# Optimization experiments

Measured on AMD Instinct MI355X. Metric: run time of the kernel, lower is better.

## Reference

```python
import jax, jax.numpy as jnp
import numpy as np
from jax import lax


def _crf_numerator(emissions, tags, mask, start_transitions, end_transitions, transitions):
    # emissions [B,S,L], tags [B,S] int, mask [B,S] bool
    B, S, L = emissions.shape
    em = jnp.take_along_axis(emissions, tags[..., None], axis=-1)[..., 0]  # [B,S]
    tr = transitions[tags[:, :-1], tags[:, 1:]]  # [B,S-1]
    m = mask.astype(emissions.dtype)
    score = start_transitions[tags[:, 0]] + em[:, 0]
    score = score + jnp.sum(m[:, 1:] * (tr + em[:, 1:]), axis=1)
    seq_len = jnp.sum(mask.astype(jnp.int32), axis=1)  # [B]
    last_tags = tags[jnp.arange(B), seq_len - 1]
    return score + end_transitions[last_tags]


def _crf_denominator(emissions, mask, start_transitions, end_transitions, transitions):
    # Forward algorithm (log-sum-exp recurrence) over time via lax.scan.
    score0 = start_transitions[None, :] + emissions[:, 0]  # [B,L]

    def step(score, inp):
        emit, m = inp  # emit [B,L], m [B] bool
        nxt = jax.nn.logsumexp(score[:, :, None] + transitions[None, :, :] + emit[:, None, :], axis=1)
        score = jnp.where(m[:, None], nxt, score)
        return score, None

    emits = jnp.swapaxes(emissions[:, 1:], 0, 1)  # [S-1,B,L]
    ms = jnp.swapaxes(mask[:, 1:], 0, 1)          # [S-1,B]
    score, _ = lax.scan(step, score0, (emits, ms))
    return jax.nn.logsumexp(score + end_transitions[None, :], axis=1)


def setup_inputs() -> dict:
    key = jax.random.key(0)
    ks = jax.random.split(key, 6)
    B, S, H, L = 32, 2048, 1024, 13
    hidden_states = jax.random.normal(ks[0], (B, S, H), jnp.float32)
    attention_mask = jnp.ones((B, S), jnp.int32)
    labels = jax.random.randint(ks[1], (B, S), 0, L, dtype=jnp.int32)
    W = jax.random.normal(ks[2], (L, H), jnp.float32) * 0.02
    b = jnp.zeros((L,), jnp.float32)
    start_transitions = jax.random.uniform(ks[3], (L,), jnp.float32, -0.1, 0.1)
    end_transitions = jax.random.uniform(ks[4], (L,), jnp.float32, -0.1, 0.1)
    transitions = jax.random.uniform(ks[5], (L, L), jnp.float32, -0.1, 0.1)
    return dict(hidden_states=hidden_states, attention_mask=attention_mask, labels=labels,
                W=W, b=b, start_transitions=start_transitions,
                end_transitions=end_transitions, transitions=transitions)


def reference(hidden_states, attention_mask, labels, W, b, start_transitions, end_transitions, transitions):
    # classifier (dropout omitted: eval mode / deterministic)
    logits = jnp.einsum('bsh,lh->bsl', hidden_states, W) + b  # [B,S,L]
    mask = attention_mask.astype(bool)
    num = _crf_numerator(logits, labels, mask, start_transitions, end_transitions, transitions)
    den = _crf_denominator(logits, mask, start_transitions, end_transitions, transitions)
    llh = num - den  # [B]
    loss = -jnp.mean(llh)  # reduction='mean', negated
    return loss, logits
```

## Files before the change

kernel.cpp:

```cpp
#include <hip/hip_runtime.h>
#include <math.h>

#define Lc 13
#define Hc 1024
#define Bc 32
#define Sc 2048
#define BSc (Bc*Sc)
#define CHUNK 128
#define NCHUNK 16
#define NBLK (Bc*NCHUNK)

#define ROWS 64
#define PW   64
#define NP   (Hc/PW)
#define THREADS 512

#define INV_LN2 1.44269504088896340736f
#define LN2f    0.69314718055994530942f

#if __has_builtin(__builtin_amdgcn_exp2f)
#define EXP2F(x) __builtin_amdgcn_exp2f(x)
#else
#define EXP2F(x) exp2f(x)
#endif
#if __has_builtin(__builtin_amdgcn_logf)
#define LOG2F(x) __builtin_amdgcn_logf(x)
#else
#define LOG2F(x) log2f(x)
#endif

__global__ __launch_bounds__(THREADS, 8)
void k_logits(const float* __restrict__ A, const float* __restrict__ W,
              const float* __restrict__ bias, float* __restrict__ out) {
  __shared__ float buf[2][ROWS * PW];
  const int tid = threadIdx.x;
  const int ln  = tid & 63;
  const int wu  = __builtin_amdgcn_readfirstlane(tid >> 6);
  const int rowBase = blockIdx.x * ROWS;

  float acc[Lc];
#pragma unroll
  for (int l = 0; l < Lc; ++l) acc[l] = 0.f;

  auto stage = [&](int p, int bsel) {
#pragma unroll
    for (int i = 0; i < 2; ++i) {
      int slot = wu * 128 + i * 64 + ln;
      int row  = slot >> 4;
      int c    = slot & 15;
      int h = ((c & 8) << 2) + ((((c & 7) ^ (row & 7))) << 2);
      const float* gp = A + (size_t)(rowBase + row) * Hc + (size_t)p * PW + h;
      float* lp = &buf[bsel][(wu * 128 + i * 64) * 4];
      __builtin_amdgcn_global_load_lds(
          (const __attribute__((address_space(1))) void*)gp,
          (__attribute__((address_space(3))) void*)lp, 16, 0, 0);
    }
  };

  stage(0, 0);
  for (int p = 0; p < NP; ++p) {
    const int cur = p & 1;
    __syncthreads();
    if (p + 1 < NP) stage(p + 1, cur ^ 1);
    const int row = ln;
#pragma unroll
    for (int j = 0; j < 2; ++j) {
      int f = wu * 8 + j * 4;
      int addr = row * PW + (f & 32) + (((((f >> 2) & 7) ^ (row & 7))) << 2);
      float4 a = *(const float4*)&buf[cur][addr];
#pragma unroll
      for (int l = 0; l < Lc; ++l) {
        const float4 wv = *(const float4*)(W + (size_t)l * Hc + (size_t)p * PW + f);
        acc[l] += a.x * wv.x + a.y * wv.y + a.z * wv.z + a.w * wv.w;
      }
    }
  }

  __syncthreads();
  float* part = &buf[0][0];
#pragma unroll
  for (int l = 0; l < Lc; ++l) part[(wu * 64 + ln) * Lc + l] = acc[l];
  __syncthreads();
  for (int o = tid; o < ROWS * Lc; o += THREADS) {
    int l = o % Lc;
    float s = bias[l];
#pragma unroll
    for (int ww = 0; ww < 8; ++ww) s += part[ww * (64 * Lc) + o];
    out[(size_t)rowBase * Lc + o] = s;
  }
}

__global__ void k_chunks(const float* __restrict__ logits, const int* __restrict__ mask,
                         const int* __restrict__ labels, const float* __restrict__ T,
                         float* __restrict__ Mout, float* __restrict__ numpart,
                         float* __restrict__ cntpart) {
  const int bp = blockIdx.x;
  const int b  = bp >> 4;
  const int p  = bp & 15;
  const int tid = threadIdx.x;
  const int g = tid >> 4;
  const int k = tid & 15;
  const int kk = (k < 13) ? k : 0;
  const int gg = (g < 13) ? g : 0;
  const bool active = (g < 13) && (k < 13);
  const size_t lbase = (size_t)b * Sc;
  const int t0 = 1 + p * CHUNK;
  const int t1 = min(t0 + CHUNK, Sc);

  float U[13];
#pragma unroll
  for (int j = 0; j < 13; ++j) U[j] = EXP2F(T[j * 13 + kk] * INV_LN2);

  float e0 = logits[(lbase + t0) * Lc + kk] * INV_LN2;
  int   m0 = mask[lbase + t0];
  float P = m0 ? EXP2F(T[gg * 13 + kk] * INV_LN2 + e0) : ((g == k) ? 1.f : 0.f);
  float off = 0.f;

  for (int t = t0 + 1; t < t1; ++t) {
    float e2 = logits[(lbase + t) * Lc + kk] * INV_LN2;
    int   mk = mask[lbase + t];
    float pj[13];
#pragma unroll
    for (int j = 0; j < 13; ++j) pj[j] = __shfl(P, j, 16);
    float s0 = pj[0] * U[0];  s0 = fmaf(pj[4],  U[4],  s0);
    s0 = fmaf(pj[8],  U[8],  s0);  s0 = fmaf(pj[12], U[12], s0);
    float s1 = pj[1] * U[1];  s1 = fmaf(pj[5],  U[5],  s1);  s1 = fmaf(pj[9],  U[9],  s1);
    float s2 = pj[2] * U[2];  s2 = fmaf(pj[6],  U[6],  s2);  s2 = fmaf(pj[10], U[10], s2);
    float s3 = pj[3] * U[3];  s3 = fmaf(pj[7],  U[7],  s3);  s3 = fmaf(pj[11], U[11], s3);
    float s = (s0 + s1) + (s2 + s3);
    float Pn = EXP2F(e2) * s;
    P = mk ? Pn : P;
    if (((t - t0) & 7) == 0) {
      float mx = P;
#pragma unroll
      for (int o = 1; o < 16; o <<= 1) mx = fmaxf(mx, __shfl_xor(mx, o, 16));
      unsigned eb = (__float_as_uint(mx) >> 23) & 255u;
      float scale = __uint_as_float((254u - eb) << 23);
      P *= scale;
      off += (float)((int)eb - 127);
    }
  }
  if (active) Mout[(size_t)bp * 169 + g * 13 + k] = (P > 0.f) ? (LOG2F(P) + off) : -1e30f;

  if (tid < 64) {
    float np = 0.f; int cnt = 0;
    for (int t = t0 + tid; t < t1; t += 64) {
      int mk = mask[lbase + t];
      if (mk) {
        int tg = labels[lbase + t];
        int pg = labels[lbase + t - 1];
        np += T[pg * 13 + tg] + logits[(lbase + t) * Lc + tg];
        cnt += 1;
      }
    }
#pragma unroll
    for (int o = 1; o < 64; o <<= 1) {
      np  += __shfl_xor(np, o, 64);
      cnt += __shfl_xor(cnt, o, 64);
    }
    if (tid == 0) { numpart[bp] = np; cntpart[bp] = (float)cnt; }
  }
}

__global__ void k_final(const float* __restrict__ logits, const int* __restrict__ mask,
                        const int* __restrict__ labels, const float* __restrict__ startT,
                        const float* __restrict__ endT, const float* __restrict__ Mws,
                        const float* __restrict__ numpart, const float* __restrict__ cntpart,
                        float* __restrict__ out0) {
  const int b = blockIdx.x;
  const int lane = threadIdx.x;
  const int kk = (lane < 13) ? lane : 0;
  const size_t lbase = (size_t)b * Sc;

  float v = (startT[kk] + logits[lbase * Lc + kk]) * INV_LN2;
  for (int p = 0; p < NCHUNK; ++p) {
    const float* Mp = Mws + (size_t)(b * NCHUNK + p) * 169;
    float a[13];
#pragma unroll
    for (int j = 0; j < 13; ++j) a[j] = __shfl(v, j, 64) + Mp[j * 13 + kk];
    float mx = a[0];
#pragma unroll
    for (int j = 1; j < 13; ++j) mx = fmaxf(mx, a[j]);
    float s = 0.f;
#pragma unroll
    for (int j = 0; j < 13; ++j) s += EXP2F(a[j] - mx);
    v = mx + LOG2F(s);
  }
  float x = (lane < 13) ? (v + endT[kk] * INV_LN2) : -1e30f;
  float mx = x;
#pragma unroll
  for (int off = 1; off < 16; off <<= 1) mx = fmaxf(mx, __shfl_xor(mx, off, 16));
  float sx = EXP2F(x - mx);
#pragma unroll
  for (int off = 1; off < 16; off <<= 1) sx += __shfl_xor(sx, off, 16);
  float den = (mx + LOG2F(sx)) * LN2f;

  float np = 0.f, cs = 0.f;
  if (lane < NCHUNK) { np = numpart[b * NCHUNK + lane]; cs = cntpart[b * NCHUNK + lane]; }
#pragma unroll
  for (int o = 1; o < 16; o <<= 1) {
    np += __shfl_xor(np, o, 16);
    cs += __shfl_xor(cs, o, 16);
  }
  if (lane == 0) {
    int lab0 = labels[lbase];
    int seqlen = mask[lbase] + (int)(cs + 0.5f);
    int lastTag = labels[lbase + seqlen - 1];
    float num = startT[lab0] + logits[lbase * Lc + lab0] + np + endT[lastTag];
    float llh = num - den;
    atomicAdd(out0, -llh * (1.0f / Bc));
  }
}

extern "C" void kernel_launch(void* const* d_in, const int* in_sizes, int n_in,
                              void* d_out, int out_size, void* d_ws, size_t ws_size,
                              hipStream_t stream) {
  const float* hs     = (const float*)d_in[0];
  const int*   amask  = (const int*)d_in[1];
  const int*   labels = (const int*)d_in[2];
  const float* W      = (const float*)d_in[3];
  const float* bias   = (const float*)d_in[4];
  const float* startT = (const float*)d_in[5];
  const float* endT   = (const float*)d_in[6];
  const float* T      = (const float*)d_in[7];

  float* out    = (float*)d_out;
  float* logits = out + 1;
  float* Mws    = (float*)d_ws;
  float* numpart = Mws + (size_t)NBLK * 169;
  float* cntpart = numpart + NBLK;

  hipMemsetAsync(d_out, 0, sizeof(float), stream);
  k_logits<<<BSc / ROWS, THREADS, 0, stream>>>(hs, W, bias, logits);
  k_chunks<<<NBLK, 256, 0, stream>>>(logits, amask, labels, T, Mws, numpart, cntpart);
  k_final <<<Bc, 64, 0, stream>>>(logits, amask, labels, startT, endT, Mws, numpart, cntpart, out);
}
```

Measured before the change: 127.6 us.

## Deepen logits GEMV pipeline to four LDS stages and drop memset launch

The hidden-state streaming kernel moves from a double-buffered 64-wide panel to a four-buffer ring of 32-wide panels. It keeps three async global-to-LDS loads in flight, using explicit vmcnt waits and a raw barrier so it no longer needs a full syncthreads per panel. The aim is to hide more memory latency on this bandwidth-bound 256MB read. Separately, the output memset is replaced by a store in the chunk kernel, which removes one launch. In exchange, each panel now needs twice as many barriers and W loads are spread over more iterations.

After: 133.9 us. 4.9% more time.

```diff
diff --git a/kernel.cpp b/kernel.cpp
--- a/kernel.cpp
+++ b/kernel.cpp
@@ -11,8 +11,9 @@
 #define NBLK (Bc*NCHUNK)
 
 #define ROWS 64
-#define PW   64
+#define PW   32
 #define NP   (Hc/PW)
+#define NBUF 4
 #define THREADS 512
 
 #define INV_LN2 1.44269504088896340736f
@@ -32,7 +33,7 @@
 __global__ __launch_bounds__(THREADS, 8)
 void k_logits(const float* __restrict__ A, const float* __restrict__ W,
               const float* __restrict__ bias, float* __restrict__ out) {
-  __shared__ float buf[2][ROWS * PW];
+  __shared__ float buf[NBUF][ROWS * PW];
   const int tid = threadIdx.x;
   const int ln  = tid & 63;
   const int wu  = __builtin_amdgcn_readfirstlane(tid >> 6);
@@ -42,38 +43,37 @@
 #pragma unroll
   for (int l = 0; l < Lc; ++l) acc[l] = 0.f;
 
-  auto stage = [&](int p, int bsel) {
-#pragma unroll
-    for (int i = 0; i < 2; ++i) {
-      int slot = wu * 128 + i * 64 + ln;
-      int row  = slot >> 4;
-      int c    = slot & 15;
-      int h = ((c & 8) << 2) + ((((c & 7) ^ (row & 7))) << 2);
-      const float* gp = A + (size_t)(rowBase + row) * Hc + (size_t)p * PW + h;
-      float* lp = &buf[bsel][(wu * 128 + i * 64) * 4];
-      __builtin_amdgcn_global_load_lds(
-          (const __attribute__((address_space(1))) void*)gp,
-          (__attribute__((address_space(3))) void*)lp, 16, 0, 0);
-    }
+  auto stage = [&](int p) {
+    int slot = wu * 64 + ln;
+    int row  = slot >> 3;
+    int c    = slot & 7;
+    int h    = (c ^ (row & 7)) << 2;
+    const float* gp = A + (size_t)(rowBase + row) * Hc + (size_t)p * PW + h;
+    float* lp = &buf[p & (NBUF - 1)][wu * 256];
+    __builtin_amdgcn_global_load_lds(
+        (const __attribute__((address_space(1))) void*)gp,
+        (__attribute__((address_space(3))) void*)lp, 16, 0, 0);
   };
 
-  stage(0, 0);
+  auto compute = [&](int p) {
+    const float* bp = &buf[p & (NBUF - 1)][0];
+    float4 a = *(const float4*)&bp[ln * PW + ((wu ^ (ln & 7)) << 2)];
+    const float* Wp = W + (size_t)p * PW + (wu << 2);
+#pragma unroll
+    for (int l = 0; l < Lc; ++l) {
+      const float4 wv = *(const float4*)(Wp + (size_t)l * Hc);
+      acc[l] += a.x * wv.x + a.y * wv.y + a.z * wv.z + a.w * wv.w;
+    }
+  };
+
+  stage(0); stage(1); stage(2);
   for (int p = 0; p < NP; ++p) {
-    const int cur = p & 1;
-    __syncthreads();
-    if (p + 1 < NP) stage(p + 1, cur ^ 1);
-    const int row = ln;
-#pragma unroll
-    for (int j = 0; j < 2; ++j) {
-      int f = wu * 8 + j * 4;
-      int addr = row * PW + (f & 32) + (((((f >> 2) & 7) ^ (row & 7))) << 2);
-      float4 a = *(const float4*)&buf[cur][addr];
-#pragma unroll
-      for (int l = 0; l < Lc; ++l) {
-        const float4 wv = *(const float4*)(W + (size_t)l * Hc + (size_t)p * PW + f);
-        acc[l] += a.x * wv.x + a.y * wv.y + a.z * wv.z + a.w * wv.w;
-      }
-    }
+    if (p < NP - 2)      asm volatile("s_waitcnt vmcnt(2)" ::: "memory");
+    else if (p == NP - 2) asm volatile("s_waitcnt vmcnt(1)" ::: "memory");
+    else                  asm volatile("s_waitcnt vmcnt(0)" ::: "memory");
+    __builtin_amdgcn_s_barrier();
+    if (p + 3 < NP) stage(p + 3);
+    compute(p);
   }
 
   __syncthreads();
@@ -93,11 +93,12 @@
 __global__ void k_chunks(const float* __restrict__ logits, const int* __restrict__ mask,
                          const int* __restrict__ labels, const float* __restrict__ T,
                          float* __restrict__ Mout, float* __restrict__ numpart,
-                         float* __restrict__ cntpart) {
+                         float* __restrict__ cntpart, float* __restrict__ out0) {
   const int bp = blockIdx.x;
   const int b  = bp >> 4;
   const int p  = bp & 15;
   const int tid = threadIdx.x;
+  if (bp == 0 && tid == 0) out0[0] = 0.f;
   const int g = tid >> 4;
   const int k = tid & 15;
   const int kk = (k < 13) ? k : 0;
@@ -230,8 +231,7 @@
   float* numpart = Mws + (size_t)NBLK * 169;
   float* cntpart = numpart + NBLK;
 
-  hipMemsetAsync(d_out, 0, sizeof(float), stream);
   k_logits<<<BSc / ROWS, THREADS, 0, stream>>>(hs, W, bias, logits);
-  k_chunks<<<NBLK, 256, 0, stream>>>(logits, amask, labels, T, Mws, numpart, cntpart);
+  k_chunks<<<NBLK, 256, 0, stream>>>(logits, amask, labels, T, Mws, numpart, cntpart, out);
   k_final <<<Bc, 64, 0, stream>>>(logits, amask, labels, startT, endT, Mws, numpart, cntpart, out);
 }
```

## Restructure logits GEMV: stage W in LDS, read A directly, reduce with DPP

Applied to the files above, without the earlier changes.

The logits kernel now loads the whole 13x1024 weight matrix into LDS once per block. Each wave streams two rows of hidden states at a time straight from global memory into registers and reduces across the wave with DPP and shuffles, replacing the old LDS staging of activations. The separate memset of the loss output is dropped; the first chunk block zeroes it instead, which saves one launch. In exchange each block pays a 52KB LDS fill, which lowers occupancy, and there are many cross-lane reduction instructions per row.

After: 380.0 us. +197.7%, slower.

```diff
diff --git a/kernel.cpp b/kernel.cpp
--- a/kernel.cpp
+++ b/kernel.cpp
@@ -9,11 +9,6 @@
 #define CHUNK 128
 #define NCHUNK 16
 #define NBLK (Bc*NCHUNK)
-
-#define ROWS 64
-#define PW   64
-#define NP   (Hc/PW)
-#define THREADS 512
 
 #define INV_LN2 1.44269504088896340736f
 #define LN2f    0.69314718055994530942f
@@ -29,75 +24,91 @@
 #define LOG2F(x) log2f(x)
 #endif
 
-__global__ __launch_bounds__(THREADS, 8)
+template <int CTRL>
+__device__ __forceinline__ float dpp_add(float v) {
+  int p = __builtin_amdgcn_update_dpp(0, __float_as_int(v), CTRL, 0xF, 0xF, true);
+  return v + __int_as_float(p);
+}
+
+__global__ __launch_bounds__(512, 4)
 void k_logits(const float* __restrict__ A, const float* __restrict__ W,
               const float* __restrict__ bias, float* __restrict__ out) {
-  __shared__ float buf[2][ROWS * PW];
+  __shared__ float Wl[Lc * Hc];
   const int tid = threadIdx.x;
-  const int ln  = tid & 63;
-  const int wu  = __builtin_amdgcn_readfirstlane(tid >> 6);
-  const int rowBase = blockIdx.x * ROWS;
-
-  float acc[Lc];
-#pragma unroll
-  for (int l = 0; l < Lc; ++l) acc[l] = 0.f;
-
-  auto stage = [&](int p, int bsel) {
-#pragma unroll
-    for (int i = 0; i < 2; ++i) {
-      int slot = wu * 128 + i * 64 + ln;
-      int row  = slot >> 4;
-      int c    = slot & 15;
-      int h = ((c & 8) << 2) + ((((c & 7) ^ (row & 7))) << 2);
-      const float* gp = A + (size_t)(rowBase + row) * Hc + (size_t)p * PW + h;
-      float* lp = &buf[bsel][(wu * 128 + i * 64) * 4];
-      __builtin_amdgcn_global_load_lds(
-          (const __attribute__((address_space(1))) void*)gp,
-          (__attribute__((address_space(3))) void*)lp, 16, 0, 0);
-    }
-  };
-
-  stage(0, 0);
-  for (int p = 0; p < NP; ++p) {
-    const int cur = p & 1;
-    __syncthreads();
-    if (p + 1 < NP) stage(p + 1, cur ^ 1);
-    const int row = ln;
-#pragma unroll
-    for (int j = 0; j < 2; ++j) {
-      int f = wu * 8 + j * 4;
-      int addr = row * PW + (f & 32) + (((((f >> 2) & 7) ^ (row & 7))) << 2);
-      float4 a = *(const float4*)&buf[cur][addr];
-#pragma unroll
-      for (int l = 0; l < Lc; ++l) {
-        const float4 wv = *(const float4*)(W + (size_t)l * Hc + (size_t)p * PW + f);
-        acc[l] += a.x * wv.x + a.y * wv.y + a.z * wv.z + a.w * wv.w;
+
+  {
+    const float4* Wg4 = (const float4*)W;
+    float4* Wl4 = (float4*)Wl;
+#pragma unroll
+    for (int i = 0; i < 7; ++i) {
+      int idx = tid + i * 512;
+      if (idx < Lc * (Hc / 4)) Wl4[idx] = Wg4[idx];
+    }
+  }
+  __syncthreads();
+
+  const int ln = tid & 63;
+  const int wv = tid >> 6;
+  const size_t rowBase = (size_t)blockIdx.x * 64 + (size_t)wv * 8;
+
+  float b[Lc];
+#pragma unroll
+  for (int l = 0; l < Lc; ++l) b[l] = bias[l];
+
+  for (int it = 0; it < 4; ++it) {
+    const size_t r0 = rowBase + (size_t)it * 2;
+    const float* A0 = A + r0 * Hc + ln * 4;
+    const float* A1 = A0 + Hc;
+    float4 a0[4], a1[4];
+#pragma unroll
+    for (int k = 0; k < 4; ++k) {
+      a0[k] = *(const float4*)(A0 + k * 256);
+      a1[k] = *(const float4*)(A1 + k * 256);
+    }
+    float acc0[Lc], acc1[Lc];
+#pragma unroll
+    for (int l = 0; l < Lc; ++l) { acc0[l] = 0.f; acc1[l] = 0.f; }
+#pragma unroll
+    for (int l = 0; l < Lc; ++l) {
+#pragma unroll
+      for (int k = 0; k < 4; ++k) {
+        float4 w = *(const float4*)&Wl[l * Hc + k * 256 + ln * 4];
+        acc0[l] = fmaf(a0[k].x, w.x, acc0[l]); acc0[l] = fmaf(a0[k].y, w.y, acc0[l]);
+        acc0[l] = fmaf(a0[k].z, w.z, acc0[l]); acc0[l] = fmaf(a0[k].w, w.w, acc0[l]);
+        acc1[l] = fmaf(a1[k].x, w.x, acc1[l]); acc1[l] = fmaf(a1[k].y, w.y, acc1[l]);
+        acc1[l] = fmaf(a1[k].z, w.z, acc1[l]); acc1[l] = fmaf(a1[k].w, w.w, acc1[l]);
       }
     }
-  }
-
-  __syncthreads();
-  float* part = &buf[0][0];
-#pragma unroll
-  for (int l = 0; l < Lc; ++l) part[(wu * 64 + ln) * Lc + l] = acc[l];
-  __syncthreads();
-  for (int o = tid; o < ROWS * Lc; o += THREADS) {
-    int l = o % Lc;
-    float s = bias[l];
-#pragma unroll
-    for (int ww = 0; ww < 8; ++ww) s += part[ww * (64 * Lc) + o];
-    out[(size_t)rowBase * Lc + o] = s;
+#pragma unroll
+    for (int l = 0; l < Lc; ++l) {
+      float s0 = acc0[l], s1 = acc1[l];
+      s0 = dpp_add<0xB1>(s0);  s1 = dpp_add<0xB1>(s1);
+      s0 = dpp_add<0x4E>(s0);  s1 = dpp_add<0x4E>(s1);
+      s0 = dpp_add<0x141>(s0); s1 = dpp_add<0x141>(s1);
+      s0 = dpp_add<0x140>(s0); s1 = dpp_add<0x140>(s1);
+      s0 += __shfl_xor(s0, 16, 64); s1 += __shfl_xor(s1, 16, 64);
+      s0 += __shfl_xor(s0, 32, 64); s1 += __shfl_xor(s1, 32, 64);
+      acc0[l] = s0; acc1[l] = s1;
+    }
+    float ov = 0.f;
+#pragma unroll
+    for (int l = 0; l < Lc; ++l) {
+      ov = (ln == l)      ? acc0[l] + b[l] : ov;
+      ov = (ln == Lc + l) ? acc1[l] + b[l] : ov;
+    }
+    if (ln < 2 * Lc) out[r0 * Lc + ln] = ov;
   }
 }
 
 __global__ void k_chunks(const float* __restrict__ logits, const int* __restrict__ mask,
                          const int* __restrict__ labels, const float* __restrict__ T,
                          float* __restrict__ Mout, float* __restrict__ numpart,
-                         float* __restrict__ cntpart) {
+                         float* __restrict__ cntpart, float* __restrict__ out0) {
   const int bp = blockIdx.x;
   const int b  = bp >> 4;
   const int p  = bp & 15;
   const int tid = threadIdx.x;
+  if (bp == 0 && tid == 0) out0[0] = 0.f;
   const int g = tid >> 4;
   const int k = tid & 15;
   const int kk = (k < 13) ? k : 0;
@@ -230,8 +241,7 @@
   float* numpart = Mws + (size_t)NBLK * 169;
   float* cntpart = numpart + NBLK;
 
-  hipMemsetAsync(d_out, 0, sizeof(float), stream);
-  k_logits<<<BSc / ROWS, THREADS, 0, stream>>>(hs, W, bias, logits);
-  k_chunks<<<NBLK, 256, 0, stream>>>(logits, amask, labels, T, Mws, numpart, cntpart);
+  k_logits<<<BSc / 64, 512, 0, stream>>>(hs, W, bias, logits);
+  k_chunks<<<NBLK, 256, 0, stream>>>(logits, amask, labels, T, Mws, numpart, cntpart, out);
   k_final <<<Bc, 64, 0, stream>>>(logits, amask, labels, startT, endT, Mws, numpart, cntpart, out);
 }
```
